# Kernel tuning notes

Hardware: AMD Instinct MI355X
Metric: run time of the kernel (lower is better)

## Reference

```python
import jax, jax.numpy as jnp
import numpy as np

B, T, E, H = 4, 2048, 1024, 16
D = E // H
SCALE = 1.0 / np.sqrt(D)


def setup_inputs() -> dict:
    key = jax.random.key(0)
    ks = jax.random.split(key, 5)
    s_in = 1.0 / np.sqrt(E)
    return {
        "x": jax.random.normal(ks[0], (B, T, E), dtype=jnp.float32),
        "W_qkv": jax.random.normal(ks[1], (E, 3 * E), dtype=jnp.float32) * s_in,
        "b_qkv": jax.random.normal(ks[2], (3 * E,), dtype=jnp.float32) * 0.02,
        "W_proj": jax.random.normal(ks[3], (E, E), dtype=jnp.float32) * s_in,
        "b_proj": jax.random.normal(ks[4], (E,), dtype=jnp.float32) * 0.02,
    }


def reference(x, W_qkv, b_qkv, W_proj, b_proj):
    Bx, Tx, _ = x.shape
    qkv = x @ W_qkv + b_qkv                      # [B, T, 3E]
    q, k, v = jnp.split(qkv, 3, axis=2)
    q = q.reshape(Bx, Tx, H, D)
    k = k.reshape(Bx, Tx, H, D)
    v = v.reshape(Bx, Tx, H, D)
    # scores [B, H, T, T]
    a = SCALE * jnp.einsum("bthd,bshd->bhts", q, k)
    causal = jnp.tril(jnp.ones((Tx, Tx), dtype=bool))
    a = jnp.where(causal, a, -jnp.inf)
    a = jax.nn.softmax(a, axis=-1)
    y = jnp.einsum("bhts,bshd->bthd", a, v).reshape(Bx, Tx, E)
    return y @ W_proj + b_proj
```

## Files before the change

kernel.cpp:

```cpp
#include <hip/hip_runtime.h>
#include <math.h>

#define Bn 4
#define Tn 2048
#define En 1024
#define Hn 16
#define Dn 64
#define RS2 (2 * En)
#define QSCALE 0.18033688f
#define SMAX 16.0f

typedef __attribute__((ext_vector_type(8))) short bfrag;
typedef __attribute__((ext_vector_type(4))) float ffrag;

__device__ __forceinline__ unsigned short f2bf(float f) {
    union { float f; unsigned int u; } v; v.f = f;
    unsigned int r = v.u + 0x7fffu + ((v.u >> 16) & 1u);
    return (unsigned short)(r >> 16);
}
__device__ __forceinline__ unsigned short f2bf_fast(float f) {
    union { float f; unsigned int u; } v; v.f = f;
    return (unsigned short)((v.u + 0x8000u) >> 16);
}

__device__ __forceinline__ void glds16(const unsigned short* g, unsigned short* l) {
    __builtin_amdgcn_global_load_lds(
        (const __attribute__((address_space(1))) unsigned int*)g,
        (__attribute__((address_space(3))) unsigned int*)l, 16, 0, 0);
}

template <int CTRL>
__device__ __forceinline__ float dpp_add_step(float x) {
    int s = __builtin_amdgcn_update_dpp(0, __builtin_bit_cast(int, x), CTRL, 0xF, 0xF, true);
    return x + __builtin_bit_cast(float, s);
}
__device__ __forceinline__ float rowsum16(float x) {
    x = dpp_add_step<0xB1>(x);
    x = dpp_add_step<0x4E>(x);
    x = dpp_add_step<0x141>(x);
    x = dpp_add_step<0x140>(x);
    return x;
}

__global__ __launch_bounds__(256) void f2bf_vec(const float* __restrict__ in,
                                                unsigned short* __restrict__ out, int n) {
    int i = (blockIdx.x * 256 + threadIdx.x) * 4;
    if (i >= n) return;
    float4 v = *(const float4*)(in + i);
    ushort4 o;
    o.x = f2bf(v.x); o.y = f2bf(v.y); o.z = f2bf(v.z); o.w = f2bf(v.w);
    *(ushort4*)(out + i) = o;
}

__global__ __launch_bounds__(256) void transpose_f2bf(const float* __restrict__ W,
                                                      unsigned short* __restrict__ Wt,
                                                      int K, int N) {
    __shared__ float s[64][65];
    const int kt = blockIdx.y * 64, nt = blockIdx.x * 64;
    const int tx = threadIdx.x & 15, ty = threadIdx.x >> 4;
#pragma unroll
    for (int i = 0; i < 4; ++i) {
        float4 v = *(const float4*)&W[(size_t)(kt + ty + i * 16) * N + nt + tx * 4];
        s[ty + i * 16][tx * 4 + 0] = v.x;
        s[ty + i * 16][tx * 4 + 1] = v.y;
        s[ty + i * 16][tx * 4 + 2] = v.z;
        s[ty + i * 16][tx * 4 + 3] = v.w;
    }
    __syncthreads();
#pragma unroll
    for (int i = 0; i < 4; ++i) {
        const int n = ty + i * 16;
        ushort4 o;
        o.x = f2bf(s[tx * 4 + 0][n]);
        o.y = f2bf(s[tx * 4 + 1][n]);
        o.z = f2bf(s[tx * 4 + 2][n]);
        o.w = f2bf(s[tx * 4 + 3][n]);
        *(ushort4*)&Wt[(size_t)(nt + n) * K + kt + tx * 4] = o;
    }
}

template <int OUT_BF16, int VSPLIT>
__global__ __launch_bounds__(256) void gemm_nt_mfma(
    const unsigned short* __restrict__ A, const unsigned short* __restrict__ Bt,
    const float* __restrict__ bias, void* __restrict__ Cv, int ldc,
    unsigned short* __restrict__ vt, int vstart,
    int M, int N, int K, int qcols, int gx)
{
    __shared__ __attribute__((aligned(16))) unsigned short As[128 * 64];
    __shared__ __attribute__((aligned(16))) unsigned short Bs[128 * 64];

    const int t = threadIdx.x;
    const int w = t >> 6, l = t & 63;
    const int wmt = (w & 1) * 4, wnt = (w >> 1) * 4;
    const int nl = l & 15, lq = l >> 4;
    const int r8 = l >> 3, c8 = l & 7;
    const int cs8 = c8 ^ r8;

    const int flat = blockIdx.x;
    const int xcd = flat & 7;
    const int g = flat >> 3;
    const int bx = g % gx;
    const int by = xcd * 8 + g / gx;
    const int m0 = by * 128, n0 = bx * 128;

    ffrag acc[4][4];
#pragma unroll
    for (int i = 0; i < 4; ++i)
#pragma unroll
        for (int j = 0; j < 4; ++j)
#pragma unroll
            for (int r = 0; r < 4; ++r) acc[i][j][r] = 0.f;

    const unsigned short* Ag = A  + (size_t)(m0 + r8) * K + cs8 * 8;
    const unsigned short* Bg = Bt + (size_t)(n0 + r8) * K + cs8 * 8;

    const int iters = K >> 6;
#pragma unroll 1
    for (int it = 0; it < iters; ++it) {
        const int k0 = it << 6;
        __syncthreads();
#pragma unroll
        for (int r = 0; r < 4; ++r) {
            const int i = w * 4 + r;
            glds16(Ag + (size_t)(i * 8) * K + k0, &As[i * 512 + l * 8]);
            glds16(Bg + (size_t)(i * 8) * K + k0, &Bs[i * 512 + l * 8]);
        }
        __syncthreads();
#pragma unroll
        for (int ks = 0; ks < 2; ++ks) {
            bfrag af[4], bf[4];
#pragma unroll
            for (int i = 0; i < 4; ++i) {
                const int pos = ((ks * 4 + lq) ^ (nl & 7)) << 3;
                af[i] = *(const bfrag*)&As[((wmt + i) * 16 + nl) * 64 + pos];
                bf[i] = *(const bfrag*)&Bs[((wnt + i) * 16 + nl) * 64 + pos];
            }
#pragma unroll
            for (int i = 0; i < 4; ++i)
#pragma unroll
                for (int j = 0; j < 4; ++j)
                    acc[i][j] = __builtin_amdgcn_mfma_f32_16x16x32_bf16(af[i], bf[j], acc[i][j], 0, 0, 0);
        }
    }

    const int orow = lq * 4, ocol = nl;
#pragma unroll
    for (int i = 0; i < 4; ++i) {
        const int gm = m0 + (wmt + i) * 16 + orow;
#pragma unroll
        for (int j = 0; j < 4; ++j) {
            const int gn = n0 + (wnt + j) * 16 + ocol;
            const float bs = bias[gn];
            if (VSPLIT && gn >= vstart) {
                const int vc = gn - vstart;
                const int b  = gm / Tn;
                const int tt = gm - b * Tn;
                ushort4 o;
                o.x = f2bf(acc[i][j][0] + bs);
                o.y = f2bf(acc[i][j][1] + bs);
                o.z = f2bf(acc[i][j][2] + bs);
                o.w = f2bf(acc[i][j][3] + bs);
                *(ushort4*)&vt[(size_t)(b * Hn * Dn + vc) * Tn + tt] = o;
            } else {
                const float sc = (qcols && gn < qcols) ? QSCALE : 1.f;
#pragma unroll
                for (int r = 0; r < 4; ++r) {
                    const float vv = (acc[i][j][r] + bs) * sc;
                    if (OUT_BF16)
                        ((unsigned short*)Cv)[(size_t)(gm + r) * ldc + gn] = f2bf(vv);
                    else
                        ((float*)Cv)[(size_t)(gm + r) * ldc + gn] = vv;
                }
            }
        }
    }
}

__global__ __launch_bounds__(256) void attn_mfma(
    const unsigned short* __restrict__ qkv,
    const unsigned short* __restrict__ vtg,
    unsigned short* __restrict__ yattn)
{
    __shared__ __attribute__((aligned(16))) unsigned short KT[128 * 64];
    __shared__ __attribute__((aligned(16))) unsigned short VT[64 * 128];
    __shared__ __attribute__((aligned(16))) unsigned short Ps[4][16][136];

    const int t = threadIdx.x;
    const int w = t >> 6, l = t & 63;
    const int nl = l & 15, lq = l >> 4;
    const int flat = blockIdx.x;
    const int bh = flat & 63;
    const int qp = flat >> 6;
    const int b = bh >> 4, h = bh & 15;

    const unsigned short* qbase = qkv + (size_t)(b * Tn) * RS2 + h * Dn;
    const unsigned short* kbase = qbase + En;
    const unsigned short* vbase = vtg + (size_t)(bh * Dn) * Tn;
    unsigned short* yb = yattn + (size_t)(b * Tn) * En + h * Dn;

#pragma unroll 1
    for (int half = 0; half < 2; ++half) {
        const int p = qp + half * 8;
#pragma unroll 1
        for (int phase = 0; phase < 2; ++phase) {
            const int qt = phase ? (31 - p) : p;
            const int rowb = qt * 64 + w * 16;
            const int jmax = qt >> 1;

            bfrag qf[2];
#pragma unroll
            for (int ks = 0; ks < 2; ++ks)
                qf[ks] = *(const bfrag*)(qbase + (size_t)(rowb + nl) * RS2 + ks * 32 + lq * 8);

            ffrag Oa[4];
            float l_i[4];
#pragma unroll
            for (int r = 0; r < 4; ++r) {
                l_i[r] = 0.f;
#pragma unroll
                for (int dt = 0; dt < 4; ++dt) Oa[dt][r] = 0.f;
            }

            for (int j = 0; j <= jmax; ++j) {
                const int k0 = j << 7;
                __syncthreads();
#pragma unroll
                for (int r = 0; r < 4; ++r) {
                    const int i = w * 4 + r;
                    glds16(kbase + (size_t)(k0 + i * 8 + (l >> 3)) * RS2 + (((l & 7) ^ (l >> 3)) << 3),
                           &KT[i * 512 + l * 8]);
                }
#pragma unroll
                for (int r = 0; r < 4; ++r) {
                    const int i = w * 4 + r;
                    const int key = ((i & 3) << 2) + (l >> 4);
                    glds16(vbase + (size_t)(i * 4 + (l >> 4)) * Tn + k0 + (((l & 15) ^ key) << 3),
                           &VT[i * 512 + l * 8]);
                }
                __syncthreads();

                ffrag s[8];
#pragma unroll
                for (int nt = 0; nt < 8; ++nt) {
                    bfrag ka = *(const bfrag*)&KT[(nt * 16 + nl) * 64 + (((lq) ^ (nl & 7)) << 3)];
                    bfrag kb = *(const bfrag*)&KT[(nt * 16 + nl) * 64 + (((4 + lq) ^ (nl & 7)) << 3)];
                    ffrag z;
#pragma unroll
                    for (int r = 0; r < 4; ++r) z[r] = -SMAX;
                    z = __builtin_amdgcn_mfma_f32_16x16x32_bf16(qf[0], ka, z, 0, 0, 0);
                    s[nt] = __builtin_amdgcn_mfma_f32_16x16x32_bf16(qf[1], kb, z, 0, 0, 0);
                }

                if (j == jmax) {
#pragma unroll
                    for (int nt = 0; nt < 8; ++nt) {
                        const int kc = k0 + nt * 16 + nl;
#pragma unroll
                        for (int r = 0; r < 4; ++r)
                            if (kc > rowb + lq * 4 + r) s[nt][r] = -INFINITY;
                    }
                }

#pragma unroll
                for (int r = 0; r < 4; ++r) {
                    const int prow = lq * 4 + r;
                    float acc = 0.f;
#pragma unroll
                    for (int nt = 0; nt < 8; ++nt) {
                        const float pvv = __builtin_amdgcn_exp2f(s[nt][r]);
                        acc += pvv;
                        Ps[w][prow][nt * 16 + nl] = f2bf_fast(pvv);
                    }
                    l_i[r] += acc;
                }

#pragma unroll
                for (int cs = 0; cs < 4; ++cs) {
                    bfrag pf = *(const bfrag*)&Ps[w][nl][cs * 32 + lq * 8];
#pragma unroll
                    for (int dt = 0; dt < 4; ++dt) {
                        bfrag vf = *(const bfrag*)&VT[(dt * 16 + nl) * 128 + ((((cs << 2) + lq) ^ nl) << 3)];
                        Oa[dt] = __builtin_amdgcn_mfma_f32_16x16x32_bf16(pf, vf, Oa[dt], 0, 0, 0);
                    }
                }
            }

#pragma unroll
            for (int r = 0; r < 4; ++r) {
                const float lr = rowsum16(l_i[r]);
                const float inv = 1.f / lr;
                const int row = rowb + lq * 4 + r;
#pragma unroll
                for (int dt = 0; dt < 4; ++dt)
                    yb[(size_t)row * En + dt * 16 + nl] = f2bf(Oa[dt][r] * inv);
            }
        }
    }
}

extern "C" void kernel_launch(void* const* d_in, const int* in_sizes, int n_in,
                              void* d_out, int out_size, void* d_ws, size_t ws_size,
                              hipStream_t stream)
{
    const float* x      = (const float*)d_in[0];
    const float* W_qkv  = (const float*)d_in[1];
    const float* b_qkv  = (const float*)d_in[2];
    const float* W_proj = (const float*)d_in[3];
    const float* b_proj = (const float*)d_in[4];
    float* out = (float*)d_out;

    const int M = Bn * Tn;
    char* ws = (char*)d_ws;
    unsigned short* xb   = (unsigned short*)ws; ws += (size_t)M * En * 2;
    unsigned short* Wqt  = (unsigned short*)ws; ws += (size_t)3 * En * En * 2;
    unsigned short* Wpt  = (unsigned short*)ws; ws += (size_t)En * En * 2;
    unsigned short* qkb  = (unsigned short*)ws; ws += (size_t)M * 2 * En * 2;
    unsigned short* vtg  = (unsigned short*)ws; ws += (size_t)M * En * 2;
    unsigned short* yb   = (unsigned short*)ws;

    f2bf_vec<<<(M * En / 4 + 255) / 256, 256, 0, stream>>>(x, xb, M * En);
    transpose_f2bf<<<dim3(3 * En / 64, En / 64), 256, 0, stream>>>(W_qkv, Wqt, En, 3 * En);
    transpose_f2bf<<<dim3(En / 64, En / 64), 256, 0, stream>>>(W_proj, Wpt, En, En);

    gemm_nt_mfma<1, 1><<<dim3((3 * En / 128) * (M / 128)), 256, 0, stream>>>(
        xb, Wqt, b_qkv, qkb, 2 * En, vtg, 2 * En, M, 3 * En, En, En, 3 * En / 128);

    attn_mfma<<<dim3(512), 256, 0, stream>>>(qkb, vtg, yb);

    gemm_nt_mfma<0, 0><<<dim3((En / 128) * (M / 128)), 256, 0, stream>>>(
        yb, Wpt, b_proj, out, En, nullptr, 1 << 30, M, En, En, 0, En / 128);
}
```

Baseline: 266.3 us.

## Keep attention P in registers via transposed QK^T MFMA and double the grid

The attention kernel now computes S^T by swapping the MFMA operands, so each lane's exp'd scores already form the A-fragment for the PV MFMA. This removes the Ps shared-memory round trip and its LDS traffic. V fragments are gathered as two 4-element reads to match the new layout. The row-sum becomes a single per-lane accumulator reduced with shuffles, and the s_setprio hints and launch bounds of 4 waves are meant to raise occupancy. The grid doubles to 1024 blocks, each handling one pair of query tiles instead of two, which changes the balance across CUs.

```diff
diff --git a/kernel.cpp b/kernel.cpp
--- a/kernel.cpp
+++ b/kernel.cpp
@@ -11,6 +11,7 @@
 #define SMAX 16.0f
 
 typedef __attribute__((ext_vector_type(8))) short bfrag;
+typedef __attribute__((ext_vector_type(4))) short sfrag4;
 typedef __attribute__((ext_vector_type(4))) float ffrag;
 
 __device__ __forceinline__ unsigned short f2bf(float f) {
@@ -27,19 +28,6 @@
     __builtin_amdgcn_global_load_lds(
         (const __attribute__((address_space(1))) unsigned int*)g,
         (__attribute__((address_space(3))) unsigned int*)l, 16, 0, 0);
-}
-
-template <int CTRL>
-__device__ __forceinline__ float dpp_add_step(float x) {
-    int s = __builtin_amdgcn_update_dpp(0, __builtin_bit_cast(int, x), CTRL, 0xF, 0xF, true);
-    return x + __builtin_bit_cast(float, s);
-}
-__device__ __forceinline__ float rowsum16(float x) {
-    x = dpp_add_step<0xB1>(x);
-    x = dpp_add_step<0x4E>(x);
-    x = dpp_add_step<0x141>(x);
-    x = dpp_add_step<0x140>(x);
-    return x;
 }
 
 __global__ __launch_bounds__(256) void f2bf_vec(const float* __restrict__ in,
@@ -176,14 +164,13 @@
     }
 }
 
-__global__ __launch_bounds__(256) void attn_mfma(
+__global__ __launch_bounds__(256, 4) void attn_mfma(
     const unsigned short* __restrict__ qkv,
     const unsigned short* __restrict__ vtg,
     unsigned short* __restrict__ yattn)
 {
     __shared__ __attribute__((aligned(16))) unsigned short KT[128 * 64];
     __shared__ __attribute__((aligned(16))) unsigned short VT[64 * 128];
-    __shared__ __attribute__((aligned(16))) unsigned short Ps[4][16][136];
 
     const int t = threadIdx.x;
     const int w = t >> 6, l = t & 63;
@@ -199,101 +186,107 @@
     unsigned short* yb = yattn + (size_t)(b * Tn) * En + h * Dn;
 
 #pragma unroll 1
-    for (int half = 0; half < 2; ++half) {
-        const int p = qp + half * 8;
-#pragma unroll 1
-        for (int phase = 0; phase < 2; ++phase) {
-            const int qt = phase ? (31 - p) : p;
-            const int rowb = qt * 64 + w * 16;
-            const int jmax = qt >> 1;
-
-            bfrag qf[2];
-#pragma unroll
-            for (int ks = 0; ks < 2; ++ks)
-                qf[ks] = *(const bfrag*)(qbase + (size_t)(rowb + nl) * RS2 + ks * 32 + lq * 8);
-
-            ffrag Oa[4];
-            float l_i[4];
+    for (int phase = 0; phase < 2; ++phase) {
+        const int qt = phase ? (31 - qp) : qp;
+        const int rowb = qt * 64 + w * 16;
+        const int jmax = qt >> 1;
+        const int qrow = rowb + nl;
+
+        bfrag qf[2];
+#pragma unroll
+        for (int ks = 0; ks < 2; ++ks)
+            qf[ks] = *(const bfrag*)(qbase + (size_t)(rowb + nl) * RS2 + ks * 32 + lq * 8);
+
+        ffrag Oa[4];
+        float li = 0.f;
+#pragma unroll
+        for (int dt = 0; dt < 4; ++dt)
+#pragma unroll
+            for (int r = 0; r < 4; ++r) Oa[dt][r] = 0.f;
+
+        for (int j = 0; j <= jmax; ++j) {
+            const int k0 = j << 7;
+            __syncthreads();
 #pragma unroll
             for (int r = 0; r < 4; ++r) {
-                l_i[r] = 0.f;
-#pragma unroll
-                for (int dt = 0; dt < 4; ++dt) Oa[dt][r] = 0.f;
-            }
-
-            for (int j = 0; j <= jmax; ++j) {
-                const int k0 = j << 7;
-                __syncthreads();
-#pragma unroll
-                for (int r = 0; r < 4; ++r) {
-                    const int i = w * 4 + r;
-                    glds16(kbase + (size_t)(k0 + i * 8 + (l >> 3)) * RS2 + (((l & 7) ^ (l >> 3)) << 3),
-                           &KT[i * 512 + l * 8]);
-                }
-#pragma unroll
-                for (int r = 0; r < 4; ++r) {
-                    const int i = w * 4 + r;
-                    const int key = ((i & 3) << 2) + (l >> 4);
-                    glds16(vbase + (size_t)(i * 4 + (l >> 4)) * Tn + k0 + (((l & 15) ^ key) << 3),
-                           &VT[i * 512 + l * 8]);
-                }
-                __syncthreads();
-
-                ffrag s[8];
-#pragma unroll
-                for (int nt = 0; nt < 8; ++nt) {
-                    bfrag ka = *(const bfrag*)&KT[(nt * 16 + nl) * 64 + (((lq) ^ (nl & 7)) << 3)];
-                    bfrag kb = *(const bfrag*)&KT[(nt * 16 + nl) * 64 + (((4 + lq) ^ (nl & 7)) << 3)];
-                    ffrag z;
-#pragma unroll
-                    for (int r = 0; r < 4; ++r) z[r] = -SMAX;
-                    z = __builtin_amdgcn_mfma_f32_16x16x32_bf16(qf[0], ka, z, 0, 0, 0);
-                    s[nt] = __builtin_amdgcn_mfma_f32_16x16x32_bf16(qf[1], kb, z, 0, 0, 0);
-                }
-
+                const int i = w * 4 + r;
+                glds16(kbase + (size_t)(k0 + i * 8 + (l >> 3)) * RS2 + (((l & 7) ^ (l >> 3)) << 3),
+                       &KT[i * 512 + l * 8]);
+            }
+#pragma unroll
+            for (int r = 0; r < 4; ++r) {
+                const int i = w * 4 + r;
+                const int key = ((i & 3) << 2) + (l >> 4);
+                glds16(vbase + (size_t)(i * 4 + (l >> 4)) * Tn + k0 + (((l & 15) ^ key) << 3),
+                       &VT[i * 512 + l * 8]);
+            }
+            __syncthreads();
+
+            bfrag pf[4];
+#pragma unroll
+            for (int cs = 0; cs < 4; ++cs) {
+                const int n0 = cs * 2, n1 = cs * 2 + 1;
+                const int pos0 = (lq ^ (nl & 7)) << 3;
+                const int pos1 = ((4 + lq) ^ (nl & 7)) << 3;
+                bfrag ka0 = *(const bfrag*)&KT[(n0 * 16 + nl) * 64 + pos0];
+                bfrag kb0 = *(const bfrag*)&KT[(n0 * 16 + nl) * 64 + pos1];
+                bfrag ka1 = *(const bfrag*)&KT[(n1 * 16 + nl) * 64 + pos0];
+                bfrag kb1 = *(const bfrag*)&KT[(n1 * 16 + nl) * 64 + pos1];
+                ffrag z0, z1;
+#pragma unroll
+                for (int r = 0; r < 4; ++r) { z0[r] = -SMAX; z1[r] = -SMAX; }
+                __builtin_amdgcn_s_setprio(1);
+                z0 = __builtin_amdgcn_mfma_f32_16x16x32_bf16(ka0, qf[0], z0, 0, 0, 0);
+                z0 = __builtin_amdgcn_mfma_f32_16x16x32_bf16(kb0, qf[1], z0, 0, 0, 0);
+                z1 = __builtin_amdgcn_mfma_f32_16x16x32_bf16(ka1, qf[0], z1, 0, 0, 0);
+                z1 = __builtin_amdgcn_mfma_f32_16x16x32_bf16(kb1, qf[1], z1, 0, 0, 0);
+                __builtin_amdgcn_s_setprio(0);
                 if (j == jmax) {
 #pragma unroll
-                    for (int nt = 0; nt < 8; ++nt) {
-                        const int kc = k0 + nt * 16 + nl;
-#pragma unroll
-                        for (int r = 0; r < 4; ++r)
-                            if (kc > rowb + lq * 4 + r) s[nt][r] = -INFINITY;
+                    for (int r = 0; r < 4; ++r) {
+                        if (k0 + n0 * 16 + lq * 4 + r > qrow) z0[r] = -INFINITY;
+                        if (k0 + n1 * 16 + lq * 4 + r > qrow) z1[r] = -INFINITY;
                     }
                 }
-
 #pragma unroll
                 for (int r = 0; r < 4; ++r) {
-                    const int prow = lq * 4 + r;
-                    float acc = 0.f;
-#pragma unroll
-                    for (int nt = 0; nt < 8; ++nt) {
-                        const float pvv = __builtin_amdgcn_exp2f(s[nt][r]);
-                        acc += pvv;
-                        Ps[w][prow][nt * 16 + nl] = f2bf_fast(pvv);
-                    }
-                    l_i[r] += acc;
+                    const float p0 = __builtin_amdgcn_exp2f(z0[r]);
+                    const float p1 = __builtin_amdgcn_exp2f(z1[r]);
+                    li += p0;
+                    li += p1;
+                    pf[cs][r]     = (short)f2bf_fast(p0);
+                    pf[cs][4 + r] = (short)f2bf_fast(p1);
                 }
-
-#pragma unroll
-                for (int cs = 0; cs < 4; ++cs) {
-                    bfrag pf = *(const bfrag*)&Ps[w][nl][cs * 32 + lq * 8];
-#pragma unroll
-                    for (int dt = 0; dt < 4; ++dt) {
-                        bfrag vf = *(const bfrag*)&VT[(dt * 16 + nl) * 128 + ((((cs << 2) + lq) ^ nl) << 3)];
-                        Oa[dt] = __builtin_amdgcn_mfma_f32_16x16x32_bf16(pf, vf, Oa[dt], 0, 0, 0);
-                    }
+            }
+
+            __builtin_amdgcn_s_setprio(1);
+#pragma unroll
+            for (int cs = 0; cs < 4; ++cs) {
+#pragma unroll
+                for (int dt = 0; dt < 4; ++dt) {
+                    const int d = dt * 16 + nl;
+                    const int base = d * 128 + ((lq & 1) << 2);
+                    const int cA = (((cs << 2) + (lq >> 1)) ^ nl) << 3;
+                    const int cB = (((cs << 2) + 2 + (lq >> 1)) ^ nl) << 3;
+                    sfrag4 va = *(const sfrag4*)&VT[base + cA];
+                    sfrag4 vb = *(const sfrag4*)&VT[base + cB];
+                    bfrag vf = __builtin_shufflevector(va, vb, 0, 1, 2, 3, 4, 5, 6, 7);
+                    Oa[dt] = __builtin_amdgcn_mfma_f32_16x16x32_bf16(pf[cs], vf, Oa[dt], 0, 0, 0);
                 }
             }
-
-#pragma unroll
-            for (int r = 0; r < 4; ++r) {
-                const float lr = rowsum16(l_i[r]);
-                const float inv = 1.f / lr;
-                const int row = rowb + lq * 4 + r;
-#pragma unroll
-                for (int dt = 0; dt < 4; ++dt)
-                    yb[(size_t)row * En + dt * 16 + nl] = f2bf(Oa[dt][r] * inv);
-            }
+            __builtin_amdgcn_s_setprio(0);
+        }
+
+        li += __shfl_xor(li, 16, 64);
+        li += __shfl_xor(li, 32, 64);
+#pragma unroll
+        for (int r = 0; r < 4; ++r) {
+            const float lr = __shfl(li, lq * 4 + r, 64);
+            const float inv = 1.f / lr;
+            const int row = rowb + lq * 4 + r;
+#pragma unroll
+            for (int dt = 0; dt < 4; ++dt)
+                yb[(size_t)row * En + dt * 16 + nl] = f2bf(Oa[dt][r] * inv);
         }
     }
 }
@@ -325,7 +318,7 @@
     gemm_nt_mfma<1, 1><<<dim3((3 * En / 128) * (M / 128)), 256, 0, stream>>>(
         xb, Wqt, b_qkv, qkb, 2 * En, vtg, 2 * En, M, 3 * En, En, En, 3 * En / 128);
 
-    attn_mfma<<<dim3(512), 256, 0, stream>>>(qkb, vtg, yb);
+    attn_mfma<<<dim3(1024), 256, 0, stream>>>(qkb, vtg, yb);
 
     gemm_nt_mfma<0, 0><<<dim3((En / 128) * (M / 128)), 256, 0, stream>>>(
         yb, Wpt, b_proj, out, En, nullptr, 1 << 30, M, En, En, 0, En / 128);
```

Measured after the change: 255.4 us. -4.1%, faster.
